# Kernel optimization log

Hardware: AMD Instinct MI355X
Metric: run time of the kernel (lower is better)

Reference implementation:

```python
import jax, jax.numpy as jnp
import numpy as np
from jax import lax

FEAT = 192   # features
GROUP = 3
B, H, W = 16, 64, 64
CIN = 2 * FEAT        # 384, input channels of x
CGATE = 4 * FEAT      # 768, gate channels


def _group_ids(C, g=GROUP):
    # contiguous channel blocks: channel c -> group c*g//C
    return (np.arange(C) * g) // C


def _mask_B(out_c, in_c, kw):
    # PixelRNN mask 'B' for a (1,kw) kernel: left-of-center columns fully
    # connected, center column obeys group rule (out_group >= in_group),
    # right-of-center columns blocked.
    og = _group_ids(out_c)[:, None]
    ig = _group_ids(in_c)[None, :]
    center = (og >= ig).astype(np.float32)  # (out_c, in_c)
    m = np.zeros((out_c, in_c, 1, kw), dtype=np.float32)
    m[:, :, :, : kw // 2] = 1.0
    m[:, :, 0, kw // 2] = center
    return jnp.asarray(m)


def _shuffle(h):
    # (B, 3*4*(F/3), H, W): group-major gate layout -> gate-major group layout
    b, c, hh, ww = h.shape
    return h.reshape(b, GROUP, 4, FEAT // GROUP, hh, ww) \
            .transpose(0, 2, 1, 3, 4, 5).reshape(b, c, hh, ww)


def setup_inputs() -> dict:
    key = jax.random.key(0)
    k1, k2, k3, k4, k5 = jax.random.split(key, 5)
    x = jax.random.normal(k1, (B, CIN, H, W), dtype=jnp.float32)
    w_i2s = jax.random.normal(k2, (CGATE, CIN, 1, 3), dtype=jnp.float32) * 0.02
    w_s2s = jax.random.normal(k3, (CGATE, FEAT, 1, 3), dtype=jnp.float32) * 0.02
    w_skip = jax.random.normal(k4, (CIN, FEAT, 1, 1), dtype=jnp.float32) * 0.05
    b_skip = jax.random.normal(k5, (CIN,), dtype=jnp.float32) * 0.01
    return {"x": x, "w_i2s": w_i2s, "w_s2s": w_s2s,
            "w_skip": w_skip, "b_skip": b_skip}


def reference(x, w_i2s, w_s2s, w_skip, b_skip):
    mask_i2s = _mask_B(CGATE, CIN, 3)
    mask_skip = _mask_B(CIN, FEAT, 1)

    # input-to-state: masked (1,3) conv, 'same' padding on width
    h = lax.conv_general_dilated(
        x, w_i2s * mask_i2s, (1, 1), ((0, 0), (1, 1)),
        dimension_numbers=("NCHW", "OIHW", "NCHW"))
    h = _shuffle(h)                       # (B, 4F, H, W)

    w1 = w_s2s[:, :, 0, :]                # (4F, F, 3) for 1D width conv
    h_rows = h.transpose(2, 0, 1, 3)      # (H, B, 4F, W)

    def step(carry, h_row):
        _h, c = carry                     # each (B, F, W)
        s = lax.conv_general_dilated(
            _h, w1, (1,), ((1, 1),),
            dimension_numbers=("NCW", "OIW", "NCW")) + h_row
        o, f, i, g = jnp.split(jax.nn.sigmoid(s), 4, axis=1)
        c = f * c + i * g
        _h = o * jnp.tanh(c)
        return (_h, c), _h

    init = (jnp.zeros((B, FEAT, W), x.dtype), jnp.zeros((B, FEAT, W), x.dtype))
    _, out_h = lax.scan(step, init, h_rows)   # (H, B, F, W)
    out_h = out_h.transpose(1, 2, 0, 3)       # (B, F, H, W)

    skip = lax.conv_general_dilated(
        out_h, w_skip * mask_skip, (1, 1), ((0, 0), (0, 0)),
        dimension_numbers=("NCHW", "OIHW", "NCHW")) + b_skip[None, :, None, None]
    return x + skip
```

## Files before the change

### kernel.cpp

```cpp
#include <hip/hip_runtime.h>
#include <hip/hip_cooperative_groups.h>
#include <cmath>

#define FEAT  192
#define CINCH 384
#define CGATE 768
#define BATCH 16
#define HH    64
#define WW    64
#define NP    (BATCH*HH*WW)
#define KI2S  768
#define KS2S  576
#define NBLK  192

using bf16   = __bf16;
using bf16x8 = __attribute__((ext_vector_type(8))) __bf16;
using bf16x4 = __attribute__((ext_vector_type(4))) __bf16;
using f32x4  = __attribute__((ext_vector_type(4))) float;
typedef unsigned long long u64;

__device__ __forceinline__ void ic_store64(u64* p, u64 v) {
    __hip_atomic_store(p, v, __ATOMIC_RELAXED, __HIP_MEMORY_SCOPE_AGENT);
}
__device__ __forceinline__ u64 ic_load64(const u64* p) {
    return __hip_atomic_load(p, __ATOMIC_RELAXED, __HIP_MEMORY_SCOPE_AGENT);
}
__device__ __forceinline__ void ic_store32(unsigned* p, unsigned v) {
    __hip_atomic_store(p, v, __ATOMIC_RELAXED, __HIP_MEMORY_SCOPE_AGENT);
}
__device__ __forceinline__ unsigned ic_load32(const unsigned* p) {
    return __hip_atomic_load(p, __ATOMIC_RELAXED, __HIP_MEMORY_SCOPE_AGENT);
}

__device__ __forceinline__ float sigm_fast(float v) {
    return __builtin_amdgcn_rcpf(1.f + __expf(-v));
}
__device__ __forceinline__ float tanh_fast(float v) {
    return 1.f - 2.f * __builtin_amdgcn_rcpf(1.f + __expf(2.f * v));
}

__global__ void pack_weights(const float* __restrict__ wi, const float* __restrict__ ws,
                             const float* __restrict__ wk,
                             bf16* __restrict__ WpA, bf16* __restrict__ WpS,
                             bf16* __restrict__ WpK) {
    int tid = blockIdx.x * 256 + threadIdx.x;
    int stride = gridDim.x * 256;
    for (int idx = tid; idx < CGATE * KI2S; idx += stride) {
        int cp = idx / KI2S, k = idx % KI2S;
        int q = cp / 192, r = cp % 192, g = r / 64, f = r % 64;
        int c = g * 256 + q * 64 + f;
        float v;
        if (k < CINCH) {
            v = wi[(c * CINCH + k) * 3 + 0];
        } else {
            int ic = k - CINCH;
            v = (g >= ic / 128) ? wi[(c * CINCH + ic) * 3 + 1] : 0.f;
        }
        WpA[idx] = (bf16)v;
    }
    for (int idx = tid; idx < CGATE * KS2S; idx += stride) {
        int oc = idx / KS2S, k = idx % KS2S;
        int t = k / FEAT, f = k % FEAT;
        WpS[idx] = (bf16)ws[(oc * FEAT + f) * 3 + t];
    }
    for (int idx = tid; idx < CINCH * FEAT; idx += stride) {
        int co = idx / FEAT, f = idx % FEAT;
        WpK[idx] = (co / 128 >= f / 64) ? (bf16)wk[idx] : (bf16)0.f;
    }
}

__global__ void pack_x(const float* __restrict__ x, bf16* __restrict__ Xp) {
    __shared__ float tile[64][65];
    int b = blockIdx.x >> 6, y = blockIdx.x & 63;
    const float* xb = x + ((size_t)b * CINCH * HH + y) * WW;
    bf16* Xrow = Xp + ((size_t)b * HH * WW + (size_t)y * WW) * KI2S;
    for (int ic0 = 0; ic0 < CINCH; ic0 += 64) {
        for (int rep = 0; rep < 16; ++rep) {
            int idx = rep * 256 + threadIdx.x;
            int i = idx >> 6, w = idx & 63;
            tile[i][w] = xb[(size_t)(ic0 + i) * (HH * WW) + w];
        }
        __syncthreads();
        for (int rep = 0; rep < 16; ++rep) {
            int idx = rep * 256 + threadIdx.x;
            int w = idx >> 6, i = idx & 63;
            Xrow[(size_t)w * KI2S + CINCH + ic0 + i] = (bf16)tile[i][w];
            Xrow[(size_t)w * KI2S + ic0 + i] = (w == 0) ? (bf16)0.f : (bf16)tile[i][w - 1];
        }
        __syncthreads();
    }
}

__global__ __launch_bounds__(256) void gemm_i2s(const bf16* __restrict__ A,
                                                const bf16* __restrict__ B,
                                                bf16* __restrict__ Hout) {
    __shared__ __align__(16) bf16 As[128 * 64];
    __shared__ __align__(16) bf16 Bs[128 * 64];
    const int m0 = blockIdx.y * 128;
    const int p0 = blockIdx.x * 128;
    const int tid = threadIdx.x;
    const int lane = tid & 63, wid = tid >> 6;
    const int quad = lane >> 4, col = lane & 15;
    const int mhalf = (wid & 1) * 64, nhalf = (wid >> 1) * 64;
    f32x4 acc[4][4] = {};
    for (int k0 = 0; k0 < KI2S; k0 += 64) {
        #pragma unroll
        for (int r = 0; r < 4; ++r) {
            int L = r * 256 + tid;
            int row = L >> 3, slot = L & 7;
            int c = slot ^ (row & 7);
            const bf16* srcA = &A[(size_t)(m0 + row) * KI2S + k0 + c * 8];
            const bf16* srcB = &B[(size_t)(p0 + row) * KI2S + k0 + c * 8];
            bf16* dstA = As + (size_t)(r * 256 + wid * 64) * 8;
            bf16* dstB = Bs + (size_t)(r * 256 + wid * 64) * 8;
            __builtin_amdgcn_global_load_lds(
                (const __attribute__((address_space(1))) void*)srcA,
                (__attribute__((address_space(3))) void*)dstA, 16, 0, 0);
            __builtin_amdgcn_global_load_lds(
                (const __attribute__((address_space(1))) void*)srcB,
                (__attribute__((address_space(3))) void*)dstB, 16, 0, 0);
        }
        __syncthreads();
        for (int kk = 0; kk < 2; ++kk) {
            bf16x8 af[4], bfv[4];
            for (int mt = 0; mt < 4; ++mt) {
                int row = mhalf + mt * 16 + col;
                int slot = (kk * 4 + quad) ^ (row & 7);
                af[mt] = *(const bf16x8*)(&As[row * 64 + slot * 8]);
            }
            for (int nt = 0; nt < 4; ++nt) {
                int row = nhalf + nt * 16 + col;
                int slot = (kk * 4 + quad) ^ (row & 7);
                bfv[nt] = *(const bf16x8*)(&Bs[row * 64 + slot * 8]);
            }
            for (int mt = 0; mt < 4; ++mt)
                for (int nt = 0; nt < 4; ++nt)
                    acc[mt][nt] = __builtin_amdgcn_mfma_f32_16x16x32_bf16(
                        af[mt], bfv[nt], acc[mt][nt], 0, 0, 0);
        }
        __syncthreads();
    }
    for (int mt = 0; mt < 4; ++mt)
        for (int nt = 0; nt < 4; ++nt) {
            int m = m0 + mhalf + mt * 16 + quad * 4;
            int p = p0 + nhalf + nt * 16 + col;
            for (int r = 0; r < 4; ++r)
                Hout[(size_t)(m + r) * NP + p] = (bf16)acc[mt][nt][r];
        }
}

__global__ __launch_bounds__(256) void scan_kernel(
    const bf16* __restrict__ Hbuf,
    const bf16* __restrict__ Ws2s,
    const bf16* __restrict__ Wskip,
    const float* __restrict__ x,
    const float* __restrict__ b_skip,
    float* __restrict__ out,
    bf16* __restrict__ hg,
    unsigned* __restrict__ cnt) {
    cooperative_groups::grid_group grid = cooperative_groups::this_grid();
    __shared__ __align__(16) bf16 hlds[66 * 200];
    __shared__ __align__(16) bf16 hnew[64 * 20];
    const int bid = blockIdx.x;
    const int b = (bid & 7) * 2 + (bid / 96);
    const int j = (bid >> 3) % 12;
    const int tid = threadIdx.x, lane = tid & 63, wid = tid >> 6;
    const int quad = lane >> 4, col = lane & 15;

    {
        const int total = 3 * 16 * 66 * 192 / 2;
        for (int i = bid * 256 + tid; i < total; i += NBLK * 256)
            ((unsigned*)hg)[i] = 0u;
        if (tid < 32) cnt[(bid % 16) * 32 + tid] = 0u;
        for (int i = tid; i < 66 * 100; i += 256) ((unsigned*)hlds)[i] = 0u;
    }
    bf16x8 Ag[18];
    {
        int f = 16 * j + wid * 4 + (col >> 2), q = col & 3;
        const bf16* Arow = Ws2s + (size_t)(q * 192 + f) * KS2S + quad * 8;
        for (int kc = 0; kc < 18; ++kc) Ag[kc] = *(const bf16x8*)(Arow + kc * 32);
    }
    bf16x8 Ak[6];
    const int mtk = wid & 1, ntk0 = (wid >> 1) * 2;
    {
        int co = 32 * j + mtk * 16 + col;
        const bf16* Krow = Wskip + (size_t)co * FEAT + quad * 8;
        for (int kc = 0; kc < 6; ++kc) Ak[kc] = *(const bf16x8*)(Krow + kc * 32);
    }
    const int fmine = 16 * j + wid * 4 + quad;
    const int lf = wid * 4 + quad;
    float cstate[4] = {0.f, 0.f, 0.f, 0.f};
    unsigned* myflags = cnt + b * 32;
    grid.sync();

    const size_t pbase = (size_t)b * HH * WW;
    float hadd[4][4];
    {
        for (int nt = 0; nt < 4; ++nt) {
            int w = nt * 16 + col;
            for (int r = 0; r < 4; ++r)
                hadd[nt][r] = (float)Hbuf[(size_t)(r * FEAT + fmine) * NP + pbase + w];
        }
    }

    for (int y = 0; y < 64; ++y) {
        f32x4 acc[4] = {};
        for (int kc = 0; kc < 18; ++kc) {
            int k0 = kc * 32 + quad * 8;
            int t = k0 / FEAT, f = k0 % FEAT;
            for (int nt = 0; nt < 4; ++nt) {
                int w = nt * 16 + col;
                bf16x8 bfr = *(const bf16x8*)(&hlds[(w + t) * 200 + f]);
                acc[nt] = __builtin_amdgcn_mfma_f32_16x16x32_bf16(Ag[kc], bfr, acc[nt], 0, 0, 0);
            }
        }
        for (int nt = 0; nt < 4; ++nt) {
            int w = nt * 16 + col;
            float so = acc[nt][0] + hadd[nt][0];
            float sf = acc[nt][1] + hadd[nt][1];
            float si = acc[nt][2] + hadd[nt][2];
            float sg = acc[nt][3] + hadd[nt][3];
            float go = sigm_fast(so);
            float gf = sigm_fast(sf);
            float gi = sigm_fast(si);
            float gg = sigm_fast(sg);
            float cc = gf * cstate[nt] + gi * gg;
            cstate[nt] = cc;
            hnew[w * 20 + lf] = (bf16)(go * tanh_fast(cc));
        }
        __syncthreads();

        {
            bf16* dst = hg + ((size_t)(y % 3) * 16 + b) * (66 * 192);
            int w = tid >> 2, fo = (tid & 3) * 4;
            u64 v = *(const u64*)(&hnew[w * 20 + fo]);
            ic_store64((u64*)(dst + (size_t)(w + 1) * 192 + 16 * j + fo), v);
        }
        __syncthreads();
        if (tid == 0) ic_store32(&myflags[j], (unsigned)(y + 1));

        if (y < 63) {
            const size_t prow = pbase + (size_t)(y + 1) * WW;
            for (int nt = 0; nt < 4; ++nt) {
                int w = nt * 16 + col;
                for (int r = 0; r < 4; ++r)
                    hadd[nt][r] = (float)Hbuf[(size_t)(r * FEAT + fmine) * NP + prow + w];
            }
        }

        if (y > 0) {
            const int ym = y - 1;
            f32x4 acc2[2] = {};
            for (int kc = 0; kc < 6; ++kc)
                for (int i = 0; i < 2; ++i) {
                    int w = (ntk0 + i) * 16 + col;
                    bf16x8 bfr = *(const bf16x8*)(&hlds[(w + 1) * 200 + kc * 32 + quad * 8]);
                    acc2[i] = __builtin_amdgcn_mfma_f32_16x16x32_bf16(Ak[kc], bfr, acc2[i], 0, 0, 0);
                }
            for (int r = 0; r < 4; ++r) {
                int co = 32 * j + mtk * 16 + quad * 4 + r;
                float bs = b_skip[co];
                for (int i = 0; i < 2; ++i) {
                    int w = (ntk0 + i) * 16 + col;
                    size_t xi = ((size_t)(b * CINCH + co) * HH + ym) * WW + w;
                    out[xi] = x[xi] + bs + acc2[i][r];
                }
            }
        }
        __syncthreads();

        {
            const unsigned tgt = (unsigned)(y + 1);
            while (true) {
                unsigned v = (lane < 12) ? ic_load32(&myflags[lane]) : tgt;
                if (__ballot(v >= tgt) == ~0ull) break;
                __builtin_amdgcn_s_sleep(1);
            }
            asm volatile("" ::: "memory");
        }

        {
            const u64* src = (const u64*)(hg + ((size_t)(y % 3) * 16 + b) * (66 * 192));
            #pragma unroll
            for (int it = 0; it < 13; ++it) {
                int c = it * 256 + tid;
                if (c < 66 * 48) {
                    u64 v = ic_load64(src + c);
                    int w = c / 48, fc = c % 48;
                    *(u64*)(&hlds[w * 200 + fc * 4]) = v;
                }
            }
        }
        __syncthreads();
    }

    {
        const int ym = 63;
        f32x4 acc2[2] = {};
        for (int kc = 0; kc < 6; ++kc)
            for (int i = 0; i < 2; ++i) {
                int w = (ntk0 + i) * 16 + col;
                bf16x8 bfr = *(const bf16x8*)(&hlds[(w + 1) * 200 + kc * 32 + quad * 8]);
                acc2[i] = __builtin_amdgcn_mfma_f32_16x16x32_bf16(Ak[kc], bfr, acc2[i], 0, 0, 0);
            }
        for (int r = 0; r < 4; ++r) {
            int co = 32 * j + mtk * 16 + quad * 4 + r;
            float bs = b_skip[co];
            for (int i = 0; i < 2; ++i) {
                int w = (ntk0 + i) * 16 + col;
                size_t xi = ((size_t)(b * CINCH + co) * HH + ym) * WW + w;
                out[xi] = x[xi] + bs + acc2[i][r];
            }
        }
    }
}

extern "C" void kernel_launch(void* const* d_in, const int* in_sizes, int n_in,
                              void* d_out, int out_size, void* d_ws, size_t ws_size,
                              hipStream_t stream) {
    const float* x      = (const float*)d_in[0];
    const float* w_i2s  = (const float*)d_in[1];
    const float* w_s2s  = (const float*)d_in[2];
    const float* w_skip = (const float*)d_in[3];
    const float* b_skip = (const float*)d_in[4];
    float* out = (float*)d_out;

    char* ws = (char*)d_ws;
    const size_t HBUF_B = (size_t)CGATE * NP * 2;
    bf16* Hbuf = (bf16*)ws;
    size_t off = HBUF_B;
    bf16* WpA  = (bf16*)(ws + off); off += (size_t)CGATE * KI2S * 2;
    bf16* WpS  = (bf16*)(ws + off); off += (size_t)CGATE * KS2S * 2;
    bf16* WpK  = (bf16*)(ws + off); off += (size_t)CINCH * FEAT * 2;
    bf16* hg   = (bf16*)(ws + off); off += (size_t)3 * 16 * 66 * 192 * 2;
    unsigned* cnt = (unsigned*)(ws + off);
    bf16* Xp   = (bf16*)d_out;

    pack_weights<<<256, 256, 0, stream>>>(w_i2s, w_s2s, w_skip, WpA, WpS, WpK);
    pack_x<<<BATCH * HH, 256, 0, stream>>>(x, Xp);
    dim3 g3(NP / 128, CGATE / 128);
    gemm_i2s<<<g3, 256, 0, stream>>>(WpA, Xp, Hbuf);

    void* args[] = { (void*)&Hbuf, (void*)&WpS, (void*)&WpK,
                     (void*)&x, (void*)&b_skip, (void*)&out, (void*)&hg, (void*)&cnt };
    hipLaunchCooperativeKernel((const void*)scan_kernel, dim3(NBLK), dim3(256),
                               args, 0, stream);
}
```

Before: 753.4 us.

## Double scan kernel block to 512 threads, splitting width tiles across waves

The recurrent scan kernel now runs 8 waves per block instead of 4. The extra waves split the width dimension, so each wave computes 2 of the 4 width tiles for the gate GEMM and 1 skip tile instead of 2. The goal is to shorten the per-row serial critical path by giving each step more parallelism. The cost is that each wave still holds its 18 weight fragments in registers, so register pressure per CU doubles and occupancy may suffer. Cooperative launch residency could also become harder.

```diff
diff --git a/kernel.cpp b/kernel.cpp
--- a/kernel.cpp
+++ b/kernel.cpp
@@ -12,6 +12,7 @@
 #define KI2S  768
 #define KS2S  576
 #define NBLK  192
+#define SCANT 512
 
 using bf16   = __bf16;
 using bf16x8 = __attribute__((ext_vector_type(8))) __bf16;
@@ -149,7 +150,7 @@
         }
 }
 
-__global__ __launch_bounds__(256) void scan_kernel(
+__global__ __launch_bounds__(SCANT) void scan_kernel(
     const bf16* __restrict__ Hbuf,
     const bf16* __restrict__ Ws2s,
     const bf16* __restrict__ Wskip,
@@ -166,71 +167,75 @@
     const int j = (bid >> 3) % 12;
     const int tid = threadIdx.x, lane = tid & 63, wid = tid >> 6;
     const int quad = lane >> 4, col = lane & 15;
+    const int wh = wid & 3;
+    const int wn = wid >> 2;
 
     {
         const int total = 3 * 16 * 66 * 192 / 2;
-        for (int i = bid * 256 + tid; i < total; i += NBLK * 256)
+        for (int i = bid * SCANT + tid; i < total; i += NBLK * SCANT)
             ((unsigned*)hg)[i] = 0u;
         if (tid < 32) cnt[(bid % 16) * 32 + tid] = 0u;
-        for (int i = tid; i < 66 * 100; i += 256) ((unsigned*)hlds)[i] = 0u;
+        for (int i = tid; i < 66 * 100; i += SCANT) ((unsigned*)hlds)[i] = 0u;
     }
     bf16x8 Ag[18];
     {
-        int f = 16 * j + wid * 4 + (col >> 2), q = col & 3;
+        int f = 16 * j + wh * 4 + (col >> 2), q = col & 3;
         const bf16* Arow = Ws2s + (size_t)(q * 192 + f) * KS2S + quad * 8;
         for (int kc = 0; kc < 18; ++kc) Ag[kc] = *(const bf16x8*)(Arow + kc * 32);
     }
     bf16x8 Ak[6];
-    const int mtk = wid & 1, ntk0 = (wid >> 1) * 2;
+    const int mtk = wid & 1, ntk = wid >> 1;
     {
         int co = 32 * j + mtk * 16 + col;
         const bf16* Krow = Wskip + (size_t)co * FEAT + quad * 8;
         for (int kc = 0; kc < 6; ++kc) Ak[kc] = *(const bf16x8*)(Krow + kc * 32);
     }
-    const int fmine = 16 * j + wid * 4 + quad;
-    const int lf = wid * 4 + quad;
-    float cstate[4] = {0.f, 0.f, 0.f, 0.f};
+    const int fmine = 16 * j + wh * 4 + quad;
+    const int lf = wh * 4 + quad;
+    float cstate[2] = {0.f, 0.f};
     unsigned* myflags = cnt + b * 32;
     grid.sync();
 
     const size_t pbase = (size_t)b * HH * WW;
-    float hadd[4][4];
-    {
-        for (int nt = 0; nt < 4; ++nt) {
-            int w = nt * 16 + col;
+    float hadd[2][4];
+    {
+        for (int i = 0; i < 2; ++i) {
+            int w = (wn * 2 + i) * 16 + col;
             for (int r = 0; r < 4; ++r)
-                hadd[nt][r] = (float)Hbuf[(size_t)(r * FEAT + fmine) * NP + pbase + w];
+                hadd[i][r] = (float)Hbuf[(size_t)(r * FEAT + fmine) * NP + pbase + w];
         }
     }
 
     for (int y = 0; y < 64; ++y) {
-        f32x4 acc[4] = {};
+        f32x4 acc[2] = {};
         for (int kc = 0; kc < 18; ++kc) {
             int k0 = kc * 32 + quad * 8;
             int t = k0 / FEAT, f = k0 % FEAT;
-            for (int nt = 0; nt < 4; ++nt) {
-                int w = nt * 16 + col;
+            #pragma unroll
+            for (int i = 0; i < 2; ++i) {
+                int w = (wn * 2 + i) * 16 + col;
                 bf16x8 bfr = *(const bf16x8*)(&hlds[(w + t) * 200 + f]);
-                acc[nt] = __builtin_amdgcn_mfma_f32_16x16x32_bf16(Ag[kc], bfr, acc[nt], 0, 0, 0);
-            }
-        }
-        for (int nt = 0; nt < 4; ++nt) {
-            int w = nt * 16 + col;
-            float so = acc[nt][0] + hadd[nt][0];
-            float sf = acc[nt][1] + hadd[nt][1];
-            float si = acc[nt][2] + hadd[nt][2];
-            float sg = acc[nt][3] + hadd[nt][3];
+                acc[i] = __builtin_amdgcn_mfma_f32_16x16x32_bf16(Ag[kc], bfr, acc[i], 0, 0, 0);
+            }
+        }
+        #pragma unroll
+        for (int i = 0; i < 2; ++i) {
+            int w = (wn * 2 + i) * 16 + col;
+            float so = acc[i][0] + hadd[i][0];
+            float sf = acc[i][1] + hadd[i][1];
+            float si = acc[i][2] + hadd[i][2];
+            float sg = acc[i][3] + hadd[i][3];
             float go = sigm_fast(so);
             float gf = sigm_fast(sf);
             float gi = sigm_fast(si);
             float gg = sigm_fast(sg);
-            float cc = gf * cstate[nt] + gi * gg;
-            cstate[nt] = cc;
+            float cc = gf * cstate[i] + gi * gg;
+            cstate[i] = cc;
             hnew[w * 20 + lf] = (bf16)(go * tanh_fast(cc));
         }
         __syncthreads();
 
-        {
+        if (tid < 256) {
             bf16* dst = hg + ((size_t)(y % 3) * 16 + b) * (66 * 192);
             int w = tid >> 2, fo = (tid & 3) * 4;
             u64 v = *(const u64*)(&hnew[w * 20 + fo]);
@@ -241,30 +246,26 @@
 
         if (y < 63) {
             const size_t prow = pbase + (size_t)(y + 1) * WW;
-            for (int nt = 0; nt < 4; ++nt) {
-                int w = nt * 16 + col;
+            #pragma unroll
+            for (int i = 0; i < 2; ++i) {
+                int w = (wn * 2 + i) * 16 + col;
                 for (int r = 0; r < 4; ++r)
-                    hadd[nt][r] = (float)Hbuf[(size_t)(r * FEAT + fmine) * NP + prow + w];
+                    hadd[i][r] = (float)Hbuf[(size_t)(r * FEAT + fmine) * NP + prow + w];
             }
         }
 
         if (y > 0) {
             const int ym = y - 1;
-            f32x4 acc2[2] = {};
-            for (int kc = 0; kc < 6; ++kc)
-                for (int i = 0; i < 2; ++i) {
-                    int w = (ntk0 + i) * 16 + col;
-                    bf16x8 bfr = *(const bf16x8*)(&hlds[(w + 1) * 200 + kc * 32 + quad * 8]);
-                    acc2[i] = __builtin_amdgcn_mfma_f32_16x16x32_bf16(Ak[kc], bfr, acc2[i], 0, 0, 0);
-                }
+            f32x4 acc2 = {};
+            int wsk = ntk * 16 + col;
+            for (int kc = 0; kc < 6; ++kc) {
+                bf16x8 bfr = *(const bf16x8*)(&hlds[(wsk + 1) * 200 + kc * 32 + quad * 8]);
+                acc2 = __builtin_amdgcn_mfma_f32_16x16x32_bf16(Ak[kc], bfr, acc2, 0, 0, 0);
+            }
             for (int r = 0; r < 4; ++r) {
                 int co = 32 * j + mtk * 16 + quad * 4 + r;
-                float bs = b_skip[co];
-                for (int i = 0; i < 2; ++i) {
-                    int w = (ntk0 + i) * 16 + col;
-                    size_t xi = ((size_t)(b * CINCH + co) * HH + ym) * WW + w;
-                    out[xi] = x[xi] + bs + acc2[i][r];
-                }
+                size_t xi = ((size_t)(b * CINCH + co) * HH + ym) * WW + wsk;
+                out[xi] = x[xi] + b_skip[co] + acc2[r];
             }
         }
         __syncthreads();
@@ -282,8 +283,8 @@
         {
             const u64* src = (const u64*)(hg + ((size_t)(y % 3) * 16 + b) * (66 * 192));
             #pragma unroll
-            for (int it = 0; it < 13; ++it) {
-                int c = it * 256 + tid;
+            for (int it = 0; it < 7; ++it) {
+                int c = it * SCANT + tid;
                 if (c < 66 * 48) {
                     u64 v = ic_load64(src + c);
                     int w = c / 48, fc = c % 48;
@@ -295,22 +296,16 @@
     }
 
     {
-        const int ym = 63;
-        f32x4 acc2[2] = {};
-        for (int kc = 0; kc < 6; ++kc)
-            for (int i = 0; i < 2; ++i) {
-                int w = (ntk0 + i) * 16 + col;
-                bf16x8 bfr = *(const bf16x8*)(&hlds[(w + 1) * 200 + kc * 32 + quad * 8]);
-                acc2[i] = __builtin_amdgcn_mfma_f32_16x16x32_bf16(Ak[kc], bfr, acc2[i], 0, 0, 0);
-            }
+        f32x4 acc2 = {};
+        int wsk = ntk * 16 + col;
+        for (int kc = 0; kc < 6; ++kc) {
+            bf16x8 bfr = *(const bf16x8*)(&hlds[(wsk + 1) * 200 + kc * 32 + quad * 8]);
+            acc2 = __builtin_amdgcn_mfma_f32_16x16x32_bf16(Ak[kc], bfr, acc2, 0, 0, 0);
+        }
         for (int r = 0; r < 4; ++r) {
             int co = 32 * j + mtk * 16 + quad * 4 + r;
-            float bs = b_skip[co];
-            for (int i = 0; i < 2; ++i) {
-                int w = (ntk0 + i) * 16 + col;
-                size_t xi = ((size_t)(b * CINCH + co) * HH + ym) * WW + w;
-                out[xi] = x[xi] + bs + acc2[i][r];
-            }
+            size_t xi = ((size_t)(b * CINCH + co) * HH + 63) * WW + wsk;
+            out[xi] = x[xi] + b_skip[co] + acc2[r];
         }
     }
 }
@@ -343,6 +338,6 @@
 
     void* args[] = { (void*)&Hbuf, (void*)&WpS, (void*)&WpK,
                      (void*)&x, (void*)&b_skip, (void*)&out, (void*)&hg, (void*)&cnt };
-    hipLaunchCooperativeKernel((const void*)scan_kernel, dim3(NBLK), dim3(256),
+    hipLaunchCooperativeKernel((const void*)scan_kernel, dim3(NBLK), dim3(SCANT),
                                args, 0, stream);
 }
```

After: 666.5 us. -11.5%, faster.
